# Kernel optimization log

Hardware: AMD Instinct MI355X
Metric: run time of the kernel (lower is better)

## Reference

```python
import jax, jax.numpy as jnp
import numpy as np

B, T, D, H, K = 4, 2048, 512, 8, 31
INNER = 2048  # dim * ff_mult
DH = D // H   # 64
EPS = 1e-5

def _ln(x, g, b):
    m = jnp.mean(x, axis=-1, keepdims=True)
    v = jnp.var(x, axis=-1, keepdims=True)
    return (x - m) * jax.lax.rsqrt(v + EPS) * g + b

def _ff(x, g, b, w1, b1, w2, b2):
    h = jax.nn.silu(_ln(x, g, b) @ w1 + b1)
    return h @ w2 + b2

def _rope_cos_sin(t, dh, theta=10000.0):
    freqs = 1.0 / theta ** (jnp.arange(0, dh, 2, dtype=jnp.float32) / dh)
    ang = jnp.arange(t, dtype=jnp.float32)[:, None] * freqs[None, :]
    return jnp.cos(ang), jnp.sin(ang)

def _rotate(x, cos, sin):
    # x: [B,T,H,DH]; complex rotation on (even, odd) pairs, matches torch view_as_complex
    xr = x.reshape(x.shape[:-1] + (DH // 2, 2))
    xe, xo = xr[..., 0], xr[..., 1]
    c, s = cos[None, :, None, :], sin[None, :, None, :]
    return jnp.stack([xe * c - xo * s, xe * s + xo * c], axis=-1).reshape(x.shape)

def setup_inputs():
    ks = iter(jax.random.split(jax.random.key(0), 16))
    w = lambda *s: jax.random.normal(next(ks), s, jnp.float32) * 0.02
    ones = lambda n: jnp.ones((n,), jnp.float32)
    zeros = lambda n: jnp.zeros((n,), jnp.float32)
    return dict(
        x=jax.random.normal(next(ks), (B, T, D), jnp.float32),
        ff1_lng=ones(D), ff1_lnb=zeros(D),
        ff1_w1=w(D, INNER), ff1_b1=zeros(INNER), ff1_w2=w(INNER, D), ff1_b2=zeros(D),
        attn_lng=ones(D), attn_lnb=zeros(D),
        wq=w(D, D), wk=w(D, D), wv=w(D, D), wo=w(D, D),
        conv_lng=ones(D), conv_lnb=zeros(D),
        pw1_w=w(D, 2 * D), pw1_b=zeros(2 * D),
        dw_w=w(D, K), dw_b=zeros(D),
        bn_g=ones(D), bn_b=zeros(D),
        pw2_w=w(D, D), pw2_b=zeros(D),
        ff2_lng=ones(D), ff2_lnb=zeros(D),
        ff2_w1=w(D, INNER), ff2_b1=zeros(INNER), ff2_w2=w(INNER, D), ff2_b2=zeros(D),
        out_lng=ones(D), out_lnb=zeros(D),
    )

def reference(x, ff1_lng, ff1_lnb, ff1_w1, ff1_b1, ff1_w2, ff1_b2,
              attn_lng, attn_lnb, wq, wk, wv, wo,
              conv_lng, conv_lnb, pw1_w, pw1_b, dw_w, dw_b, bn_g, bn_b, pw2_w, pw2_b,
              ff2_lng, ff2_lnb, ff2_w1, ff2_b1, ff2_w2, ff2_b2,
              out_lng, out_lnb):
    # ff1 half-step
    x = x + 0.5 * _ff(x, ff1_lng, ff1_lnb, ff1_w1, ff1_b1, ff1_w2, ff1_b2)
    # RoPE MHSA
    h = _ln(x, attn_lng, attn_lnb)
    q = (h @ wq).reshape(B, T, H, DH)
    k = (h @ wk).reshape(B, T, H, DH)
    v = (h @ wv).reshape(B, T, H, DH)
    cos, sin = _rope_cos_sin(T, DH)
    q, k = _rotate(q, cos, sin), _rotate(k, cos, sin)
    scores = jnp.einsum('bqhd,bkhd->bhqk', q, k) / np.float32(np.sqrt(DH))
    o = jnp.einsum('bhqk,bkhd->bqhd', jax.nn.softmax(scores, axis=-1), v).reshape(B, T, D)
    x = x + o @ wo
    # Conformer conv module
    h = _ln(x, conv_lng, conv_lnb) @ pw1_w + pw1_b         # pointwise1 -> [B,T,2D]
    h = h[..., :D] * jax.nn.sigmoid(h[..., D:])            # GLU over channels
    h = h.transpose(0, 2, 1)                               # [B,D,T]
    h = jax.lax.conv_general_dilated(h, dw_w[:, None, :], (1,), [(K // 2, K // 2)],
                                     dimension_numbers=('NCH', 'OIH', 'NCH'),
                                     feature_group_count=D) + dw_b[None, :, None]
    mu = jnp.mean(h, axis=(0, 2), keepdims=True)           # training-mode BatchNorm1d
    var = jnp.var(h, axis=(0, 2), keepdims=True)
    h = (h - mu) * jax.lax.rsqrt(var + EPS) * bn_g[None, :, None] + bn_b[None, :, None]
    h = jax.nn.silu(h).transpose(0, 2, 1) @ pw2_w + pw2_b  # pointwise2 -> [B,T,D]
    x = x + h
    # ff2 half-step + final LN
    x = x + 0.5 * _ff(x, ff2_lng, ff2_lnb, ff2_w1, ff2_b1, ff2_w2, ff2_b2)
    return _ln(x, out_lng, out_lnb)
```

## Files before the change

### kernel.cpp

```cpp
#include <hip/hip_runtime.h>


typedef float  f32x4   __attribute__((ext_vector_type(4)));
typedef float  f32x16  __attribute__((ext_vector_type(16)));
typedef __bf16 bf16_t;
typedef __bf16 bf16x8  __attribute__((ext_vector_type(8)));
typedef unsigned short u16;
typedef unsigned short u16x4 __attribute__((ext_vector_type(4)));
typedef unsigned short u16x8 __attribute__((ext_vector_type(8)));
typedef unsigned int   u32x4 __attribute__((ext_vector_type(4)));

#define DEVI __device__ __forceinline__

static constexpr int CB = 4, CT = 2048, CD = 512, CH = 8, CDH = 64, CINNER = 2048, CK = 31;
static constexpr int CBT = CB * CT;

DEVI u16 f2bf(float f) {
  unsigned u = __builtin_bit_cast(unsigned, f);
  u += 0x7FFFu + ((u >> 16) & 1u);
  return (u16)(u >> 16);
}
DEVI float bf2f(u16 h) { return __builtin_bit_cast(float, (unsigned)h << 16); }
DEVI float sigm(float x) { return 1.0f / (1.0f + __expf(-x)); }

#if defined(__has_builtin)
#if __has_builtin(__builtin_amdgcn_exp2f)
#define FEX2(x) __builtin_amdgcn_exp2f(x)
#endif
#endif
#ifndef FEX2
DEVI float fex2_asm(float x) {
  float r;
  asm("v_exp_f32 %0, %1\n\ts_nop 1" : "=v"(r) : "v"(x));
  return r;
}
#define FEX2(x) fex2_asm(x)
#endif

DEVI unsigned cvtpk(float lo, float hi) {
  unsigned r;
  asm("v_cvt_pk_bf16_f32 %0, %1, %2" : "=v"(r) : "v"(lo), "v"(hi));
  return r;
}

DEVI void gload16(const bf16_t* g, bf16_t* l) {
  __builtin_amdgcn_global_load_lds(
      (const __attribute__((address_space(1))) unsigned int*)g,
      (__attribute__((address_space(3))) unsigned int*)l, 16, 0, 0);
}

DEVI void pipe_wait(int t, int nt) {
  if (t + 3 <= nt)      asm volatile("s_waitcnt vmcnt(12)" ::: "memory");
  else if (t + 2 == nt) asm volatile("s_waitcnt vmcnt(6)" ::: "memory");
  else                  asm volatile("s_waitcnt vmcnt(0)" ::: "memory");
}

enum { EPI_BF = 0, EPI_SILU_BF = 1, EPI_RES = 2, EPI_GLU = 3, EPI_QKV = 4, EPI_RESF = 5 };

template<int EPI>
__global__ __launch_bounds__(512) void gemm8(
    const bf16_t* __restrict__ A, const bf16_t* __restrict__ B,
    const float* __restrict__ bias, const float* __restrict__ res,
    void* __restrict__ Cv,
    int lda, int ldb, int ldc, int Kd, float scale)
{
  __shared__ __align__(16) bf16_t As[3][256 * 64];
  __shared__ __align__(16) bf16_t Bs[3][128 * 64];

  const int gx = gridDim.x;
  const int nwg = gx * gridDim.y;
  int wg = blockIdx.y * gx + blockIdx.x;
  wg = (wg & 7) * (nwg >> 3) + (wg >> 3);
  const int m0 = (wg / gx) * 256, n0 = (wg % gx) * 128;

  const int tid = threadIdx.x;
  const int wid = tid >> 6, lane = tid & 63;
  const int lrow = lane & 15, lk = lane >> 4;
  const int wm = (wid >> 1) * 64, wn = (wid & 1) * 64;
  const int r = tid >> 3;
  const int cs = (((tid & 7) ^ (r & 7)) << 3);
  const int fsw = lrow & 7;

  auto stage = [&](int kt, int s) {
    const bf16_t* ga = A + (long)(m0 + r) * lda + (kt * 64 + cs);
    const bf16_t* gb = B + (long)(n0 + r) * ldb + (kt * 64 + cs);
    bf16_t* as = &As[s][0];
    bf16_t* bs = &Bs[s][0];
#pragma unroll
    for (int it = 0; it < 4; ++it)
      gload16(ga + (long)it * 64 * lda, as + tid * 8 + it * 4096);
#pragma unroll
    for (int it = 0; it < 2; ++it)
      gload16(gb + (long)it * 64 * ldb, bs + tid * 8 + it * 4096);
  };

  f32x4 acc[4][4] = {};
  const int nt = Kd / 64;

  stage(0, 0);
  stage(1, 1);
  stage(2, 2);

  int s = 0;
  for (int t = 0; t < nt; ++t) {
    pipe_wait(t, nt);
    asm volatile("s_barrier" ::: "memory");

    bf16x8 av[2][4], bv[2][4];
    const bf16_t* as = &As[s][0];
    const bf16_t* bs = &Bs[s][0];
#pragma unroll
    for (int kk = 0; kk < 2; ++kk) {
#pragma unroll
      for (int i = 0; i < 4; ++i)
        av[kk][i] = *(const bf16x8*)&as[(wm + i * 16 + lrow) * 64 + ((((kk << 2) + lk) ^ fsw) << 3)];
#pragma unroll
      for (int j = 0; j < 4; ++j)
        bv[kk][j] = *(const bf16x8*)&bs[(wn + j * 16 + lrow) * 64 + ((((kk << 2) + lk) ^ fsw) << 3)];
    }
    __builtin_amdgcn_s_setprio(1);
#pragma unroll
    for (int kk = 0; kk < 2; ++kk)
#pragma unroll
      for (int i = 0; i < 4; ++i)
#pragma unroll
        for (int j = 0; j < 4; ++j)
          acc[i][j] = __builtin_amdgcn_mfma_f32_16x16x32_bf16(av[kk][i], bv[kk][j], acc[i][j], 0, 0, 0);
    __builtin_amdgcn_s_setprio(0);

    asm volatile("s_barrier" ::: "memory");
    if (t + 3 < nt) stage(t + 3, s);
    s = (s == 2) ? 0 : s + 1;
  }

  if constexpr (EPI == EPI_GLU) {
#pragma unroll
    for (int jp = 0; jp < 2; ++jp) {
      int oc = ((n0 + wn) >> 1) + jp * 16 + lrow;
      float ba = bias[oc], bb = bias[512 + oc];
#pragma unroll
      for (int i = 0; i < 4; ++i) {
#pragma unroll
        for (int rr = 0; rr < 4; ++rr) {
          int row = m0 + wm + i * 16 + lk * 4 + rr;
          float av_ = acc[i][2 * jp][rr] + ba;
          float bv_ = acc[i][2 * jp + 1][rr] + bb;
          ((bf16_t*)Cv)[(long)row * ldc + oc] = (bf16_t)(av_ * sigm(bv_));
        }
      }
    }
  } else if constexpr (EPI == EPI_QKV) {
    bf16_t* vt = (bf16_t*)res;
    const float2* cst = (const float2*)bias;
    const float SC = 0.125f * 1.44269504089f;
#pragma unroll
    for (int j = 0; j < 4; ++j) {
      int col = n0 + wn + j * 16 + lrow;
      if (col < 1024) {
        int ip = (col & 63) >> 1;
        bool odd = (col & 1) != 0;
        bool isQ = col < 512;
#pragma unroll
        for (int i = 0; i < 4; ++i) {
#pragma unroll
          for (int rr = 0; rr < 4; ++rr) {
            int row = m0 + wm + i * 16 + lk * 4 + rr;
            float2 csv = cst[(row & (CT - 1)) * 32 + ip];
            float mine = acc[i][j][rr];
            float other = __shfl_xor(mine, 1);
            float v = odd ? (other * csv.y + mine * csv.x)
                          : (mine * csv.x - other * csv.y);
            if (isQ) v *= SC;
            ((bf16_t*)Cv)[(long)row * ldc + col] = (bf16_t)v;
          }
        }
      } else {
        int dg = col - 1024;
        int hh = dg >> 6, d = dg & 63;
#pragma unroll
        for (int i = 0; i < 4; ++i) {
          int row0 = m0 + wm + i * 16 + lk * 4;
          int b = row0 >> 11, t = row0 & 2047;
          u16x4 pk;
#pragma unroll
          for (int rr = 0; rr < 4; ++rr) pk[rr] = f2bf(acc[i][j][rr]);
          *(u16x4*)(vt + ((long)(b * 8 + hh) * 64 + d) * 2048 + t) = pk;
        }
      }
    }
  } else {
#pragma unroll
    for (int j = 0; j < 4; ++j) {
      int col = n0 + wn + j * 16 + lrow;
      float bb = bias ? bias[col] : 0.0f;
#pragma unroll
      for (int i = 0; i < 4; ++i) {
#pragma unroll
        for (int rr = 0; rr < 4; ++rr) {
          int row = m0 + wm + i * 16 + lk * 4 + rr;
          long idx = (long)row * ldc + col;
          float v = (acc[i][j][rr] + bb) * scale;
          if constexpr (EPI == EPI_SILU_BF) v *= sigm(v);
          ((bf16_t*)Cv)[idx] = (bf16_t)v;
        }
      }
    }
  }
}

template<int BM, int BN, int BK, int EPI>
__global__ __launch_bounds__(256) void gemm_bf(
    const bf16_t* __restrict__ A, const bf16_t* __restrict__ B,
    const float* __restrict__ bias, const float* __restrict__ res,
    void* __restrict__ Cv,
    int lda, int ldb, int ldc, int Kd, float scale)
{
  __shared__ __align__(16) bf16_t As[BM * BK];
  __shared__ __align__(16) bf16_t Bs[BN * BK];

  const int gx = gridDim.x;
  const int nwg = gx * gridDim.y;
  int wg = blockIdx.y * gx + blockIdx.x;
  wg = (wg & 7) * (nwg >> 3) + (wg >> 3);
  const int m0 = (wg / gx) * BM, n0 = (wg % gx) * BN;

  const int tid = threadIdx.x;
  const int wid = tid >> 6, lane = tid & 63;
  const int lrow = lane & 15, lk = lane >> 4;
  constexpr int FM = BM / 32, FN = BN / 32;
  constexpr int NK = BK / 32;
  constexpr int TPR = BK / 8;
  constexpr int RPP = 256 / TPR;
  const int wm = (wid >> 1) * (BM / 2), wn = (wid & 1) * (BN / 2);
  const int r = tid / TPR;
  const int cs = (((tid & (TPR - 1)) ^ (r & 7)) << 3);
  const int fsw = lrow & 7;

  f32x4 acc[FM][FN] = {};

  for (int k0 = 0; k0 < Kd; k0 += BK) {
    const bf16_t* ga = A + (long)(m0 + r) * lda + (k0 + cs);
    const bf16_t* gb = B + (long)(n0 + r) * ldb + (k0 + cs);
#pragma unroll
    for (int it = 0; it < BM / RPP; ++it)
      gload16(ga + (long)it * RPP * lda, &As[tid * 8 + it * 2048]);
#pragma unroll
    for (int it = 0; it < BN / RPP; ++it)
      gload16(gb + (long)it * RPP * ldb, &Bs[tid * 8 + it * 2048]);
    __syncthreads();

    bf16x8 av[NK][FM], bv[NK][FN];
#pragma unroll
    for (int kk = 0; kk < NK; ++kk) {
#pragma unroll
      for (int i = 0; i < FM; ++i)
        av[kk][i] = *(const bf16x8*)&As[(wm + i * 16 + lrow) * BK + ((((kk << 2) + lk) ^ fsw) << 3)];
#pragma unroll
      for (int j = 0; j < FN; ++j)
        bv[kk][j] = *(const bf16x8*)&Bs[(wn + j * 16 + lrow) * BK + ((((kk << 2) + lk) ^ fsw) << 3)];
    }
#pragma unroll
    for (int kk = 0; kk < NK; ++kk)
#pragma unroll
      for (int i = 0; i < FM; ++i)
#pragma unroll
        for (int j = 0; j < FN; ++j)
          acc[i][j] = __builtin_amdgcn_mfma_f32_16x16x32_bf16(av[kk][i], bv[kk][j], acc[i][j], 0, 0, 0);
    __syncthreads();
  }

#pragma unroll
  for (int j = 0; j < FN; ++j) {
    int col = n0 + wn + j * 16 + lrow;
    float bb = bias ? bias[col] : 0.0f;
#pragma unroll
    for (int i = 0; i < FM; ++i) {
#pragma unroll
      for (int rr = 0; rr < 4; ++rr) {
        int row = m0 + wm + i * 16 + lk * 4 + rr;
        long idx = (long)row * ldc + col;
        float v = (acc[i][j][rr] + bb) * scale;
        if constexpr (EPI == EPI_SILU_BF) v *= sigm(v);
        if constexpr (EPI == EPI_RES) {
          ((bf16_t*)Cv)[idx] = (bf16_t)(bf2f(((const u16*)res)[idx]) + v);
        } else if constexpr (EPI == EPI_RESF) {
          ((bf16_t*)Cv)[idx] = (bf16_t)(res[idx] + v);
        } else {
          ((bf16_t*)Cv)[idx] = (bf16_t)v;
        }
      }
    }
  }
}

__global__ __launch_bounds__(512) void fattn_k(
    const bf16_t* __restrict__ QK,
    const bf16_t* __restrict__ VT,
    bf16_t* __restrict__ O)
{
  __shared__ __align__(16) bf16_t S[32768];

  const int tid = threadIdx.x;
  const int w = tid >> 6, lane = tid & 63;
  const int l31 = lane & 31, hi = lane >> 5;
  const int q0 = blockIdx.x * 256;
  const int bh = blockIdx.y, b = bh >> 3, h = bh & 7;

  const int r8 = tid >> 3;
  const int csw = ((tid & 7) ^ (r8 & 7)) << 3;
  const int fswl = l31 & 7;

  const bf16_t* Qg = QK + ((long)b * CT + q0) * 1536 + h * 64;
  const bf16_t* Kg = QK + (long)b * CT * 1536 + 512 + h * 64;
  const bf16_t* Vg = VT + (long)bh * 64 * 2048;

#pragma unroll
  for (int it = 0; it < 4; ++it)
    gload16(Qg + (long)(r8 + it * 64) * 1536 + csw, &S[16384 + tid * 8 + it * 4096]);
  gload16(Kg + (long)r8 * 1536 + csw, &S[tid * 8]);
  gload16(Vg + (long)r8 * 2048 + csw, &S[4096 + tid * 8]);
  __syncthreads();

  bf16x8 qb[4];
#pragma unroll
  for (int m = 0; m < 4; ++m)
    qb[m] = *(const bf16x8*)&S[16384 + (w * 32 + l31) * 64 + (((m * 2 + hi) ^ fswl) << 3)];

  const u16x8 onesu = {0x3F80, 0x3F80, 0x3F80, 0x3F80, 0x3F80, 0x3F80, 0x3F80, 0x3F80};
  const bf16x8 onesf = __builtin_bit_cast(bf16x8, onesu);

  f32x16 o0 = {}, o1 = {}, lacc = {};

#define FA_BODY(CURK, CURV, NXTK, NXTV, KV0, STG)                               \
  {                                                                             \
    if (STG) {                                                                  \
      const int nxt = (KV0) + 64;                                               \
      gload16(Kg + (long)(nxt + r8) * 1536 + csw, &S[(NXTK) + tid * 8]);        \
      gload16(Vg + (long)r8 * 2048 + nxt + csw, &S[(NXTV) + tid * 8]);          \
    }                                                                           \
    bf16x8 ka[2][4];                                                            \
    _Pragma("unroll")                                                           \
    for (int j = 0; j < 2; ++j)                                                 \
      _Pragma("unroll")                                                         \
      for (int m = 0; m < 4; ++m)                                               \
        ka[j][m] = *(const bf16x8*)&S[(CURK) + (j * 32 + l31) * 64 +            \
                                      (((m * 2 + hi) ^ fswl) << 3)];            \
    f32x16 s0 = {}, s1 = {};                                                    \
    __builtin_amdgcn_s_setprio(1);                                              \
    _Pragma("unroll")                                                           \
    for (int m = 0; m < 4; ++m) {                                               \
      s0 = __builtin_amdgcn_mfma_f32_32x32x16_bf16(ka[0][m], qb[m], s0, 0, 0, 0); \
      s1 = __builtin_amdgcn_mfma_f32_32x32x16_bf16(ka[1][m], qb[m], s1, 0, 0, 0); \
    }                                                                           \
    __builtin_amdgcn_s_setprio(0);                                              \
    _Pragma("unroll")                                                           \
    for (int rr = 0; rr < 16; ++rr) s0[rr] = FEX2(s0[rr]);                      \
    _Pragma("unroll")                                                           \
    for (int rr = 0; rr < 16; ++rr) s1[rr] = FEX2(s1[rr]);                      \
    bf16x8 pw[4];                                                               \
    _Pragma("unroll")                                                           \
    for (int jk = 0; jk < 4; ++jk) {                                            \
      float e0, e1, e2, e3, e4, e5, e6, e7;                                     \
      if (jk == 0) { e0=s0[0];e1=s0[1];e2=s0[2];e3=s0[3];e4=s0[4];e5=s0[5];e6=s0[6];e7=s0[7]; }        \
      else if (jk == 1) { e0=s0[8];e1=s0[9];e2=s0[10];e3=s0[11];e4=s0[12];e5=s0[13];e6=s0[14];e7=s0[15]; } \
      else if (jk == 2) { e0=s1[0];e1=s1[1];e2=s1[2];e3=s1[3];e4=s1[4];e5=s1[5];e6=s1[6];e7=s1[7]; }   \
      else { e0=s1[8];e1=s1[9];e2=s1[10];e3=s1[11];e4=s1[12];e5=s1[13];e6=s1[14];e7=s1[15]; }          \
      unsigned a0 = cvtpk(e0, e1), a1 = cvtpk(e2, e3);                          \
      unsigned b0 = cvtpk(e4, e5), b1 = cvtpk(e6, e7);                          \
      asm("v_permlane32_swap_b32 %0, %1" : "+v"(a0), "+v"(b0));                 \
      asm("v_permlane32_swap_b32 %0, %1" : "+v"(a1), "+v"(b1));                 \
      u32x4 t; t[0] = a0; t[1] = a1; t[2] = b0; t[3] = b1;                      \
      pw[jk] = __builtin_bit_cast(bf16x8, t);                                   \
    }                                                                           \
    bf16x8 va[2][4];                                                            \
    _Pragma("unroll")                                                           \
    for (int n = 0; n < 2; ++n)                                                 \
      _Pragma("unroll")                                                         \
      for (int jk = 0; jk < 4; ++jk)                                            \
        va[n][jk] = *(const bf16x8*)&S[(CURV) + (n * 32 + l31) * 64 +           \
                                       (((jk * 2 + hi) ^ fswl) << 3)];          \
    __builtin_amdgcn_s_setprio(1);                                              \
    _Pragma("unroll")                                                           \
    for (int jk = 0; jk < 4; ++jk) {                                            \
      o0 = __builtin_amdgcn_mfma_f32_32x32x16_bf16(va[0][jk], pw[jk], o0, 0, 0, 0); \
      o1 = __builtin_amdgcn_mfma_f32_32x32x16_bf16(va[1][jk], pw[jk], o1, 0, 0, 0); \
      lacc = __builtin_amdgcn_mfma_f32_32x32x16_bf16(onesf, pw[jk], lacc, 0, 0, 0); \
    }                                                                           \
    __builtin_amdgcn_s_setprio(0);                                              \
    __syncthreads();                                                            \
  }

  for (int kv0 = 0; kv0 < CT; kv0 += 128) {
    FA_BODY(0, 4096, 8192, 12288, kv0, 1)
    FA_BODY(8192, 12288, 0, 4096, kv0 + 64, (kv0 + 128 < CT))
  }
#undef FA_BODY

  float rl = 1.0f / lacc[0];
  bf16_t* Op = O + ((long)b * CT + q0 + w * 32 + l31) * CD + h * 64;
#pragma unroll
  for (int n = 0; n < 2; ++n) {
#pragma unroll
    for (int m = 0; m < 4; ++m) {
      u16x4 pk4;
#pragma unroll
      for (int e = 0; e < 4; ++e)
        pk4[e] = f2bf((n ? o1[m * 4 + e] : o0[m * 4 + e]) * rl);
      *(u16x4*)(Op + n * 32 + m * 8 + hi * 4) = pk4;
    }
  }
}

DEVI void wtrans_dev(const float* w, u16* o, int Kd, int N, int bx, int by,
                     int tid, u16 (*lt)[72])
{
  const int k0 = by * 64, n0 = bx * 64;
#pragma unroll
  for (int it = 0; it < 4; ++it) {
    int kk = (tid >> 4) + it * 16, nn = (tid & 15) * 4;
    float4 f = *(const float4*)(w + (long)(k0 + kk) * N + n0 + nn);
    lt[kk][nn + 0] = f2bf(f.x); lt[kk][nn + 1] = f2bf(f.y);
    lt[kk][nn + 2] = f2bf(f.z); lt[kk][nn + 3] = f2bf(f.w);
  }
  __syncthreads();
#pragma unroll
  for (int it = 0; it < 2; ++it) {
    int nn = (tid >> 3) + it * 32, kk = (tid & 7) * 8;
    u16x8 pk;
#pragma unroll
    for (int e = 0; e < 8; ++e) pk[e] = lt[kk + e][nn];
    *(u16x8*)(o + (long)(n0 + nn) * Kd + k0 + kk) = pk;
  }
}

DEVI void pwtrans_dev(const float* w, u16* o, int bx, int by, int tid,
                      u16 (*lt)[72])
{
  const int k0 = by * 64, n0 = bx * 64;
#pragma unroll
  for (int it = 0; it < 4; ++it) {
    int kk = (tid >> 4) + it * 16, nn = (tid & 15) * 4;
    float4 f = *(const float4*)(w + (long)(k0 + kk) * 1024 + n0 + nn);
    lt[kk][nn + 0] = f2bf(f.x); lt[kk][nn + 1] = f2bf(f.y);
    lt[kk][nn + 2] = f2bf(f.z); lt[kk][nn + 3] = f2bf(f.w);
  }
  __syncthreads();
#pragma unroll
  for (int it = 0; it < 2; ++it) {
    int nn = (tid >> 3) + it * 32, kk = (tid & 7) * 8;
    int s = n0 + nn;
    int d = ((s & 511) >> 4) * 32 + (s >> 9) * 16 + (s & 15);
    u16x8 pk;
#pragma unroll
    for (int e = 0; e < 8; ++e) pk[e] = lt[kk + e][nn];
    *(u16x8*)(o + (long)d * 512 + k0 + kk) = pk;
  }
}

__global__ __launch_bounds__(256) void prep_k(
    const float* ff1_w1, const float* ff1_w2,
    const float* wq, const float* wk, const float* wv, const float* wo,
    const float* pw1_w, const float* pw2_w,
    const float* ff2_w1, const float* ff2_w2, const float* dw_w,
    u16* w_ff1a, u16* w_ff1b, u16* w_qkv, u16* w_o, u16* w_pw1, u16* w_pw2,
    u16* w_ff2a, u16* w_ff2b, float* dwT, float2* ropeT)
{
  __shared__ u16 lt[64][72];
  const int r = blockIdx.x;
  const int tid = threadIdx.x;

  if (r < 256) {
    wtrans_dev(ff1_w1, w_ff1a, 512, 2048, r & 31, r >> 5, tid, lt);
  } else if (r < 512) {
    int r2 = r - 256;
    wtrans_dev(ff1_w2, w_ff1b, 2048, 512, r2 & 7, r2 >> 3, tid, lt);
  } else if (r < 576) {
    int r2 = r - 512;
    wtrans_dev(wq, w_qkv, 512, 512, r2 & 7, r2 >> 3, tid, lt);
  } else if (r < 640) {
    int r2 = r - 576;
    wtrans_dev(wk, w_qkv + (size_t)512 * 512, 512, 512, r2 & 7, r2 >> 3, tid, lt);
  } else if (r < 704) {
    int r2 = r - 640;
    wtrans_dev(wv, w_qkv + (size_t)1024 * 512, 512, 512, r2 & 7, r2 >> 3, tid, lt);
  } else if (r < 768) {
    int r2 = r - 704;
    wtrans_dev(wo, w_o, 512, 512, r2 & 7, r2 >> 3, tid, lt);
  } else if (r < 896) {
    int r2 = r - 768;
    pwtrans_dev(pw1_w, w_pw1, r2 & 15, r2 >> 4, tid, lt);
  } else if (r < 960) {
    int r2 = r - 896;
    wtrans_dev(pw2_w, w_pw2, 512, 512, r2 & 7, r2 >> 3, tid, lt);
  } else if (r < 1216) {
    int r2 = r - 960;
    wtrans_dev(ff2_w1, w_ff2a, 512, 2048, r2 & 31, r2 >> 5, tid, lt);
  } else if (r < 1472) {
    int r2 = r - 1216;
    wtrans_dev(ff2_w2, w_ff2b, 2048, 512, r2 & 7, r2 >> 3, tid, lt);
  } else if (r < 1534) {
    int i = (r - 1472) * 256 + tid;
    if (i < 512 * 31) { int c = i / 31, k = i % 31; dwT[k * 512 + c] = dw_w[i]; }
  } else {
    int i = (r - 1534) * 256 + tid;
    int t = i >> 5, ip = i & 31;
    float freq = __expf(-(float)ip * (9.210340371976184f / 32.0f));
    float ang = (float)t * freq;
    ropeT[i] = make_float2(cosf(ang), sinf(ang));
  }
}

template<int IBF, int OBF>
__global__ __launch_bounds__(256) void ln_k(
    const void* __restrict__ in, const float* __restrict__ g,
    const float* __restrict__ b, void* __restrict__ out)
{
  const int w = threadIdx.x >> 6, lane = threadIdx.x & 63;
  const long row = (long)blockIdx.x * 4 + w;
  float v[8];
  if (IBF) {
    u16x8 u = ((const u16x8*)in)[row * 64 + lane];
#pragma unroll
    for (int e = 0; e < 8; ++e) v[e] = bf2f(u[e]);
  } else {
    float4 f0 = ((const float4*)in)[row * 128 + lane * 2];
    float4 f1 = ((const float4*)in)[row * 128 + lane * 2 + 1];
    v[0] = f0.x; v[1] = f0.y; v[2] = f0.z; v[3] = f0.w;
    v[4] = f1.x; v[5] = f1.y; v[6] = f1.z; v[7] = f1.w;
  }
  float s = 0, q = 0;
#pragma unroll
  for (int e = 0; e < 8; ++e) { s += v[e]; q += v[e] * v[e]; }
#pragma unroll
  for (int o = 32; o; o >>= 1) { s += __shfl_xor(s, o); q += __shfl_xor(q, o); }
  float mean = s * (1.0f / CD);
  float var = q * (1.0f / CD) - mean * mean;
  float rstd = rsqrtf(var + 1e-5f);
  float4 g0 = ((const float4*)g)[lane * 2], g1 = ((const float4*)g)[lane * 2 + 1];
  float4 b0 = ((const float4*)b)[lane * 2], b1 = ((const float4*)b)[lane * 2 + 1];
  float gg[8] = {g0.x, g0.y, g0.z, g0.w, g1.x, g1.y, g1.z, g1.w};
  float bb[8] = {b0.x, b0.y, b0.z, b0.w, b1.x, b1.y, b1.z, b1.w};
  float o8[8];
#pragma unroll
  for (int e = 0; e < 8; ++e) o8[e] = (v[e] - mean) * rstd * gg[e] + bb[e];
  if (OBF) {
    u16x8 pk;
#pragma unroll
    for (int e = 0; e < 8; ++e) pk[e] = f2bf(o8[e]);
    ((u16x8*)out)[row * 64 + lane] = pk;
  } else {
    ((float4*)out)[row * 128 + lane * 2] = make_float4(o8[0], o8[1], o8[2], o8[3]);
    ((float4*)out)[row * 128 + lane * 2 + 1] = make_float4(o8[4], o8[5], o8[6], o8[7]);
  }
}

__global__ __launch_bounds__(256) void dwconv_k(
    const u16* __restrict__ in, const float* __restrict__ wT,
    const float* __restrict__ wb, u16* __restrict__ out)
{
  long idx = (long)blockIdx.x * 256 + threadIdx.x;
  int c4 = (int)(idx & 127) * 4;
  int t0 = (int)((idx >> 7) & 255) * 8;
  int b = (int)(idx >> 15);
  const u16* base = in + (long)b * CT * CD;
  float4 bias = *(const float4*)(wb + c4);
  float4 acc[8];
#pragma unroll
  for (int t = 0; t < 8; ++t) acc[t] = bias;
#pragma unroll
  for (int j = 0; j < 38; ++j) {
    int tr = t0 + j - 15;
    float4 row = make_float4(0.f, 0.f, 0.f, 0.f);
    if (tr >= 0 && tr < CT) {
      u16x4 rv = *(const u16x4*)(base + (long)tr * CD + c4);
      row = make_float4(bf2f(rv[0]), bf2f(rv[1]), bf2f(rv[2]), bf2f(rv[3]));
    }
#pragma unroll
    for (int t = 0; t < 8; ++t) {
      int k = j - t;
      if (k >= 0 && k < CK) {
        float4 w4 = *(const float4*)(wT + k * CD + c4);
        acc[t].x += row.x * w4.x; acc[t].y += row.y * w4.y;
        acc[t].z += row.z * w4.z; acc[t].w += row.w * w4.w;
      }
    }
  }
#pragma unroll
  for (int t = 0; t < 8; ++t) {
    u16x4 pk;
    pk[0] = f2bf(acc[t].x); pk[1] = f2bf(acc[t].y);
    pk[2] = f2bf(acc[t].z); pk[3] = f2bf(acc[t].w);
    *(u16x4*)(out + ((long)b * CT + t0 + t) * CD + c4) = pk;
  }
}

__global__ __launch_bounds__(256) void bn_part_k(
    const u16* __restrict__ in, float* __restrict__ psum, float* __restrict__ psq)
{
  const int blk = blockIdx.x;
  const int tid = threadIdx.x;
  const int c0 = tid, c1 = tid + 256;
  const int rows = CBT / 256;
  const u16* base = in + (long)blk * rows * CD;
  float s0 = 0, q0 = 0, s1 = 0, q1 = 0;
  for (int r = 0; r < rows; ++r) {
    float v0 = bf2f(base[(long)r * CD + c0]); s0 += v0; q0 += v0 * v0;
    float v1 = bf2f(base[(long)r * CD + c1]); s1 += v1; q1 += v1 * v1;
  }
  psum[blk * CD + c0] = s0; psq[blk * CD + c0] = q0;
  psum[blk * CD + c1] = s1; psq[blk * CD + c1] = q1;
}

__global__ __launch_bounds__(256) void bn_fin_k(
    const float* __restrict__ psum, const float* __restrict__ psq,
    float* __restrict__ stat)
{
  int c = blockIdx.x * 256 + threadIdx.x;
  float s = 0, q = 0;
  for (int i = 0; i < 256; ++i) { s += psum[i * CD + c]; q += psq[i * CD + c]; }
  float mean = s * (1.0f / CBT);
  float var = q * (1.0f / CBT) - mean * mean;
  stat[c] = mean;
  stat[CD + c] = rsqrtf(var + 1e-5f);
}

__global__ __launch_bounds__(256) void bn_app_k(
    const u16* __restrict__ h, const float* __restrict__ stat,
    const float* __restrict__ g, const float* __restrict__ b,
    u16* __restrict__ out)
{
  long idx = (long)blockIdx.x * 256 + threadIdx.x;
  int c = (int)(idx & 511);
  float v = (bf2f(h[idx]) - stat[c]) * stat[CD + c] * g[c] + b[c];
  v = v * sigm(v);
  out[idx] = f2bf(v);
}

extern "C" void kernel_launch(void* const* d_in, const int* in_sizes, int n_in,
                              void* d_out, int out_size, void* d_ws, size_t ws_size,
                              hipStream_t stream)
{
  const float* x        = (const float*)d_in[0];
  const float* ff1_lng  = (const float*)d_in[1];
  const float* ff1_lnb  = (const float*)d_in[2];
  const float* ff1_w1   = (const float*)d_in[3];
  const float* ff1_b1   = (const float*)d_in[4];
  const float* ff1_w2   = (const float*)d_in[5];
  const float* ff1_b2   = (const float*)d_in[6];
  const float* attn_lng = (const float*)d_in[7];
  const float* attn_lnb = (const float*)d_in[8];
  const float* wq       = (const float*)d_in[9];
  const float* wk       = (const float*)d_in[10];
  const float* wv       = (const float*)d_in[11];
  const float* wo       = (const float*)d_in[12];
  const float* conv_lng = (const float*)d_in[13];
  const float* conv_lnb = (const float*)d_in[14];
  const float* pw1_w    = (const float*)d_in[15];
  const float* pw1_b    = (const float*)d_in[16];
  const float* dw_w     = (const float*)d_in[17];
  const float* dw_b     = (const float*)d_in[18];
  const float* bn_g     = (const float*)d_in[19];
  const float* bn_b     = (const float*)d_in[20];
  const float* pw2_w    = (const float*)d_in[21];
  const float* pw2_b    = (const float*)d_in[22];
  const float* ff2_lng  = (const float*)d_in[23];
  const float* ff2_lnb  = (const float*)d_in[24];
  const float* ff2_w1   = (const float*)d_in[25];
  const float* ff2_b1   = (const float*)d_in[26];
  const float* ff2_w2   = (const float*)d_in[27];
  const float* ff2_b2   = (const float*)d_in[28];
  const float* out_lng  = (const float*)d_in[29];
  const float* out_lnb  = (const float*)d_in[30];
  float* out = (float*)d_out;

  char* p = (char*)d_ws;
  auto alloc = [&](size_t bytes) { char* r = p; p += (bytes + 255) & ~(size_t)255; return r; };
  bf16_t* bufX   = (bf16_t*)alloc((size_t)CBT * CD * 2);
  bf16_t* bufH   = (bf16_t*)alloc((size_t)CBT * CD * 2);
  bf16_t* bufQKV = (bf16_t*)alloc((size_t)CBT * 1536 * 2);
  bf16_t* bufO   = (bf16_t*)alloc((size_t)CBT * CD * 2);
  bf16_t* bufVT  = (bf16_t*)alloc((size_t)CBT * CD * 2);
  bf16_t* bufP   = (bf16_t*)alloc((size_t)CBT * CINNER * 2);
  bf16_t* w_ff1a = (bf16_t*)alloc((size_t)CD * CINNER * 2);
  bf16_t* w_ff1b = (bf16_t*)alloc((size_t)CD * CINNER * 2);
  bf16_t* w_qkv  = (bf16_t*)alloc((size_t)CD * 1536 * 2);
  bf16_t* w_o    = (bf16_t*)alloc((size_t)CD * CD * 2);
  bf16_t* w_pw1  = (bf16_t*)alloc((size_t)CD * 2 * CD * 2);
  bf16_t* w_pw2  = (bf16_t*)alloc((size_t)CD * CD * 2);
  bf16_t* w_ff2a = (bf16_t*)alloc((size_t)CD * CINNER * 2);
  bf16_t* w_ff2b = (bf16_t*)alloc((size_t)CD * CINNER * 2);
  float* dwT  = (float*)alloc((size_t)CK * CD * 4);
  float2* ropeT = (float2*)alloc((size_t)CT * 32 * 8);
  float* psum = (float*)alloc((size_t)256 * CD * 4);
  float* psq  = (float*)alloc((size_t)256 * CD * 4);
  float* stat = (float*)alloc((size_t)2 * CD * 4);

  const dim3 blk(256);
  const dim3 blk8(512);

  prep_k<<<dim3(1790), blk, 0, stream>>>(
      ff1_w1, ff1_w2, wq, wk, wv, wo, pw1_w, pw2_w, ff2_w1, ff2_w2, dw_w,
      (u16*)w_ff1a, (u16*)w_ff1b, (u16*)w_qkv, (u16*)w_o, (u16*)w_pw1,
      (u16*)w_pw2, (u16*)w_ff2a, (u16*)w_ff2b, dwT, ropeT);

  ln_k<0, 1><<<dim3(CBT / 4), blk, 0, stream>>>(x, ff1_lng, ff1_lnb, bufH);
  gemm8<EPI_SILU_BF><<<dim3(16, 32), blk8, 0, stream>>>(
      bufH, w_ff1a, ff1_b1, nullptr, bufP, CD, CD, CINNER, CD, 1.0f);
  gemm_bf<64, 128, 128, EPI_RESF><<<dim3(4, 128), blk, 0, stream>>>(
      bufP, w_ff1b, ff1_b2, x, bufX, CINNER, CINNER, CD, CINNER, 0.5f);

  ln_k<1, 1><<<dim3(CBT / 4), blk, 0, stream>>>(bufX, attn_lng, attn_lnb, bufH);
  gemm8<EPI_QKV><<<dim3(12, 32), blk8, 0, stream>>>(
      bufH, w_qkv, (const float*)ropeT, (const float*)bufVT, bufQKV, CD, CD, 1536, CD, 1.0f);
  fattn_k<<<dim3(CT / 256, CB * CH), blk8, 0, stream>>>(bufQKV, bufVT, bufO);
  gemm_bf<64, 128, 128, EPI_RES><<<dim3(4, 128), blk, 0, stream>>>(
      bufO, w_o, nullptr, (const float*)bufX, bufX, CD, CD, CD, CD, 1.0f);

  ln_k<1, 1><<<dim3(CBT / 4), blk, 0, stream>>>(bufX, conv_lng, conv_lnb, bufH);
  gemm8<EPI_GLU><<<dim3(8, 32), blk8, 0, stream>>>(
      bufH, w_pw1, pw1_b, nullptr, bufH, CD, CD, CD, CD, 1.0f);
  dwconv_k<<<dim3(512), blk, 0, stream>>>((const u16*)bufH, dwT, dw_b, (u16*)bufO);
  bn_part_k<<<dim3(256), blk, 0, stream>>>((const u16*)bufO, psum, psq);
  bn_fin_k<<<dim3(2), blk, 0, stream>>>(psum, psq, stat);
  bn_app_k<<<dim3(CBT * CD / 256), blk, 0, stream>>>((const u16*)bufO, stat, bn_g, bn_b, (u16*)bufH);
  gemm_bf<64, 128, 128, EPI_RES><<<dim3(4, 128), blk, 0, stream>>>(
      bufH, w_pw2, pw2_b, (const float*)bufX, bufX, CD, CD, CD, CD, 1.0f);

  ln_k<1, 1><<<dim3(CBT / 4), blk, 0, stream>>>(bufX, ff2_lng, ff2_lnb, bufH);
  gemm8<EPI_SILU_BF><<<dim3(16, 32), blk8, 0, stream>>>(
      bufH, w_ff2a, ff2_b1, nullptr, bufP, CD, CD, CINNER, CD, 1.0f);
  gemm_bf<64, 128, 128, EPI_RES><<<dim3(4, 128), blk, 0, stream>>>(
      bufP, w_ff2b, ff2_b2, (const float*)bufX, bufX, CINNER, CINNER, CD, CINNER, 0.5f);

  ln_k<1, 0><<<dim3(CBT / 4), blk, 0, stream>>>(bufX, out_lng, out_lnb, out);

  (void)in_sizes; (void)n_in; (void)out_size; (void)ws_size;
}
```

Before: 322.7 us.

## Replace N=512 GEMMs with 128x128 triple-buffered pipelined kernel; widen dwconv

The single-stage gemm_bf used for the four N=512 projections (ff down-projections, attention output, pw2) is replaced by gemm4n, a 512-thread, 128x128-tile kernel with a three-stage global_load_lds pipeline, vmcnt-based waits and MFMA priority boosting, mirroring the existing gemm8. The aim is to hide global-load latency that the old load-sync-compute loop exposed. The grid halves to 256 workgroups, which may reduce occupancy or wave balance on the GPU. Separately, the depthwise conv processes 8 channels per thread with 16-byte loads and stores instead of 4, halving its grid and raising register use.

```diff
diff --git a/kernel.cpp b/kernel.cpp
--- a/kernel.cpp
+++ b/kernel.cpp
@@ -49,9 +49,14 @@
       (__attribute__((address_space(3))) unsigned int*)l, 16, 0, 0);
 }
 
-DEVI void pipe_wait(int t, int nt) {
+DEVI void pipe_wait6(int t, int nt) {
   if (t + 3 <= nt)      asm volatile("s_waitcnt vmcnt(12)" ::: "memory");
   else if (t + 2 == nt) asm volatile("s_waitcnt vmcnt(6)" ::: "memory");
+  else                  asm volatile("s_waitcnt vmcnt(0)" ::: "memory");
+}
+DEVI void pipe_wait4(int t, int nt) {
+  if (t + 3 <= nt)      asm volatile("s_waitcnt vmcnt(8)" ::: "memory");
+  else if (t + 2 == nt) asm volatile("s_waitcnt vmcnt(4)" ::: "memory");
   else                  asm volatile("s_waitcnt vmcnt(0)" ::: "memory");
 }
 
@@ -103,7 +108,7 @@
 
   int s = 0;
   for (int t = 0; t < nt; ++t) {
-    pipe_wait(t, nt);
+    pipe_wait6(t, nt);
     asm volatile("s_barrier" ::: "memory");
 
     bf16x8 av[2][4], bv[2][4];
@@ -208,79 +213,91 @@
   }
 }
 
-template<int BM, int BN, int BK, int EPI>
-__global__ __launch_bounds__(256) void gemm_bf(
+template<int EPI>
+__global__ __launch_bounds__(512) void gemm4n(
     const bf16_t* __restrict__ A, const bf16_t* __restrict__ B,
     const float* __restrict__ bias, const float* __restrict__ res,
     void* __restrict__ Cv,
     int lda, int ldb, int ldc, int Kd, float scale)
 {
-  __shared__ __align__(16) bf16_t As[BM * BK];
-  __shared__ __align__(16) bf16_t Bs[BN * BK];
+  __shared__ __align__(16) bf16_t As[3][128 * 64];
+  __shared__ __align__(16) bf16_t Bs[3][128 * 64];
 
   const int gx = gridDim.x;
   const int nwg = gx * gridDim.y;
   int wg = blockIdx.y * gx + blockIdx.x;
   wg = (wg & 7) * (nwg >> 3) + (wg >> 3);
-  const int m0 = (wg / gx) * BM, n0 = (wg % gx) * BN;
+  const int m0 = (wg / gx) * 128, n0 = (wg % gx) * 128;
 
   const int tid = threadIdx.x;
   const int wid = tid >> 6, lane = tid & 63;
   const int lrow = lane & 15, lk = lane >> 4;
-  constexpr int FM = BM / 32, FN = BN / 32;
-  constexpr int NK = BK / 32;
-  constexpr int TPR = BK / 8;
-  constexpr int RPP = 256 / TPR;
-  const int wm = (wid >> 1) * (BM / 2), wn = (wid & 1) * (BN / 2);
-  const int r = tid / TPR;
-  const int cs = (((tid & (TPR - 1)) ^ (r & 7)) << 3);
+  const int wm = (wid >> 1) * 32, wn = (wid & 1) * 64;
+  const int r = tid >> 3;
+  const int cs = (((tid & 7) ^ (r & 7)) << 3);
   const int fsw = lrow & 7;
 
-  f32x4 acc[FM][FN] = {};
-
-  for (int k0 = 0; k0 < Kd; k0 += BK) {
-    const bf16_t* ga = A + (long)(m0 + r) * lda + (k0 + cs);
-    const bf16_t* gb = B + (long)(n0 + r) * ldb + (k0 + cs);
-#pragma unroll
-    for (int it = 0; it < BM / RPP; ++it)
-      gload16(ga + (long)it * RPP * lda, &As[tid * 8 + it * 2048]);
-#pragma unroll
-    for (int it = 0; it < BN / RPP; ++it)
-      gload16(gb + (long)it * RPP * ldb, &Bs[tid * 8 + it * 2048]);
-    __syncthreads();
-
-    bf16x8 av[NK][FM], bv[NK][FN];
-#pragma unroll
-    for (int kk = 0; kk < NK; ++kk) {
-#pragma unroll
-      for (int i = 0; i < FM; ++i)
-        av[kk][i] = *(const bf16x8*)&As[(wm + i * 16 + lrow) * BK + ((((kk << 2) + lk) ^ fsw) << 3)];
-#pragma unroll
-      for (int j = 0; j < FN; ++j)
-        bv[kk][j] = *(const bf16x8*)&Bs[(wn + j * 16 + lrow) * BK + ((((kk << 2) + lk) ^ fsw) << 3)];
-    }
-#pragma unroll
-    for (int kk = 0; kk < NK; ++kk)
-#pragma unroll
-      for (int i = 0; i < FM; ++i)
-#pragma unroll
-        for (int j = 0; j < FN; ++j)
+  auto stage = [&](int kt, int s) {
+    const bf16_t* ga = A + (long)(m0 + r) * lda + (kt * 64 + cs);
+    const bf16_t* gb = B + (long)(n0 + r) * ldb + (kt * 64 + cs);
+#pragma unroll
+    for (int it = 0; it < 2; ++it)
+      gload16(ga + (long)it * 64 * lda, &As[s][tid * 8 + it * 4096]);
+#pragma unroll
+    for (int it = 0; it < 2; ++it)
+      gload16(gb + (long)it * 64 * ldb, &Bs[s][tid * 8 + it * 4096]);
+  };
+
+  f32x4 acc[2][4] = {};
+  const int nt = Kd / 64;
+
+  stage(0, 0);
+  stage(1, 1);
+  stage(2, 2);
+
+  int s = 0;
+  for (int t = 0; t < nt; ++t) {
+    pipe_wait4(t, nt);
+    asm volatile("s_barrier" ::: "memory");
+
+    bf16x8 av[2][2], bv[2][4];
+    const bf16_t* as = &As[s][0];
+    const bf16_t* bs = &Bs[s][0];
+#pragma unroll
+    for (int kk = 0; kk < 2; ++kk) {
+#pragma unroll
+      for (int i = 0; i < 2; ++i)
+        av[kk][i] = *(const bf16x8*)&as[(wm + i * 16 + lrow) * 64 + ((((kk << 2) + lk) ^ fsw) << 3)];
+#pragma unroll
+      for (int j = 0; j < 4; ++j)
+        bv[kk][j] = *(const bf16x8*)&bs[(wn + j * 16 + lrow) * 64 + ((((kk << 2) + lk) ^ fsw) << 3)];
+    }
+    __builtin_amdgcn_s_setprio(1);
+#pragma unroll
+    for (int kk = 0; kk < 2; ++kk)
+#pragma unroll
+      for (int i = 0; i < 2; ++i)
+#pragma unroll
+        for (int j = 0; j < 4; ++j)
           acc[i][j] = __builtin_amdgcn_mfma_f32_16x16x32_bf16(av[kk][i], bv[kk][j], acc[i][j], 0, 0, 0);
-    __syncthreads();
-  }
-
-#pragma unroll
-  for (int j = 0; j < FN; ++j) {
+    __builtin_amdgcn_s_setprio(0);
+
+    asm volatile("s_barrier" ::: "memory");
+    if (t + 3 < nt) stage(t + 3, s);
+    s = (s == 2) ? 0 : s + 1;
+  }
+
+#pragma unroll
+  for (int j = 0; j < 4; ++j) {
     int col = n0 + wn + j * 16 + lrow;
     float bb = bias ? bias[col] : 0.0f;
 #pragma unroll
-    for (int i = 0; i < FM; ++i) {
+    for (int i = 0; i < 2; ++i) {
 #pragma unroll
       for (int rr = 0; rr < 4; ++rr) {
         int row = m0 + wm + i * 16 + lk * 4 + rr;
         long idx = (long)row * ldc + col;
         float v = (acc[i][j][rr] + bb) * scale;
-        if constexpr (EPI == EPI_SILU_BF) v *= sigm(v);
         if constexpr (EPI == EPI_RES) {
           ((bf16_t*)Cv)[idx] = (bf16_t)(bf2f(((const u16*)res)[idx]) + v);
         } else if constexpr (EPI == EPI_RESF) {
@@ -559,38 +576,46 @@
     const float* __restrict__ wb, u16* __restrict__ out)
 {
   long idx = (long)blockIdx.x * 256 + threadIdx.x;
-  int c4 = (int)(idx & 127) * 4;
-  int t0 = (int)((idx >> 7) & 255) * 8;
-  int b = (int)(idx >> 15);
+  int c8 = (int)(idx & 63) * 8;
+  int t0 = (int)((idx >> 6) & 255) * 8;
+  int b = (int)(idx >> 14);
   const u16* base = in + (long)b * CT * CD;
-  float4 bias = *(const float4*)(wb + c4);
-  float4 acc[8];
-#pragma unroll
-  for (int t = 0; t < 8; ++t) acc[t] = bias;
+  float bias8[8];
+#pragma unroll
+  for (int e = 0; e < 8; ++e) bias8[e] = wb[c8 + e];
+  float acc[8][8];
+#pragma unroll
+  for (int t = 0; t < 8; ++t)
+#pragma unroll
+    for (int e = 0; e < 8; ++e) acc[t][e] = bias8[e];
 #pragma unroll
   for (int j = 0; j < 38; ++j) {
     int tr = t0 + j - 15;
-    float4 row = make_float4(0.f, 0.f, 0.f, 0.f);
+    float row[8];
     if (tr >= 0 && tr < CT) {
-      u16x4 rv = *(const u16x4*)(base + (long)tr * CD + c4);
-      row = make_float4(bf2f(rv[0]), bf2f(rv[1]), bf2f(rv[2]), bf2f(rv[3]));
+      u16x8 rv = *(const u16x8*)(base + (long)tr * CD + c8);
+#pragma unroll
+      for (int e = 0; e < 8; ++e) row[e] = bf2f(rv[e]);
+    } else {
+#pragma unroll
+      for (int e = 0; e < 8; ++e) row[e] = 0.0f;
     }
 #pragma unroll
     for (int t = 0; t < 8; ++t) {
       int k = j - t;
       if (k >= 0 && k < CK) {
-        float4 w4 = *(const float4*)(wT + k * CD + c4);
-        acc[t].x += row.x * w4.x; acc[t].y += row.y * w4.y;
-        acc[t].z += row.z * w4.z; acc[t].w += row.w * w4.w;
+        const float* wr = wT + k * CD + c8;
+#pragma unroll
+        for (int e = 0; e < 8; ++e) acc[t][e] += row[e] * wr[e];
       }
     }
   }
 #pragma unroll
   for (int t = 0; t < 8; ++t) {
-    u16x4 pk;
-    pk[0] = f2bf(acc[t].x); pk[1] = f2bf(acc[t].y);
-    pk[2] = f2bf(acc[t].z); pk[3] = f2bf(acc[t].w);
-    *(u16x4*)(out + ((long)b * CT + t0 + t) * CD + c4) = pk;
+    u16x8 pk;
+#pragma unroll
+    for (int e = 0; e < 8; ++e) pk[e] = f2bf(acc[t][e]);
+    *(u16x8*)(out + ((long)b * CT + t0 + t) * CD + c8) = pk;
   }
 }
 
@@ -706,30 +731,30 @@
   ln_k<0, 1><<<dim3(CBT / 4), blk, 0, stream>>>(x, ff1_lng, ff1_lnb, bufH);
   gemm8<EPI_SILU_BF><<<dim3(16, 32), blk8, 0, stream>>>(
       bufH, w_ff1a, ff1_b1, nullptr, bufP, CD, CD, CINNER, CD, 1.0f);
-  gemm_bf<64, 128, 128, EPI_RESF><<<dim3(4, 128), blk, 0, stream>>>(
+  gemm4n<EPI_RESF><<<dim3(4, 64), blk8, 0, stream>>>(
       bufP, w_ff1b, ff1_b2, x, bufX, CINNER, CINNER, CD, CINNER, 0.5f);
 
   ln_k<1, 1><<<dim3(CBT / 4), blk, 0, stream>>>(bufX, attn_lng, attn_lnb, bufH);
   gemm8<EPI_QKV><<<dim3(12, 32), blk8, 0, stream>>>(
       bufH, w_qkv, (const float*)ropeT, (const float*)bufVT, bufQKV, CD, CD, 1536, CD, 1.0f);
   fattn_k<<<dim3(CT / 256, CB * CH), blk8, 0, stream>>>(bufQKV, bufVT, bufO);
-  gemm_bf<64, 128, 128, EPI_RES><<<dim3(4, 128), blk, 0, stream>>>(
+  gemm4n<EPI_RES><<<dim3(4, 64), blk8, 0, stream>>>(
       bufO, w_o, nullptr, (const float*)bufX, bufX, CD, CD, CD, CD, 1.0f);
 
   ln_k<1, 1><<<dim3(CBT / 4), blk, 0, stream>>>(bufX, conv_lng, conv_lnb, bufH);
   gemm8<EPI_GLU><<<dim3(8, 32), blk8, 0, stream>>>(
       bufH, w_pw1, pw1_b, nullptr, bufH, CD, CD, CD, CD, 1.0f);
-  dwconv_k<<<dim3(512), blk, 0, stream>>>((const u16*)bufH, dwT, dw_b, (u16*)bufO);
+  dwconv_k<<<dim3(256), blk, 0, stream>>>((const u16*)bufH, dwT, dw_b, (u16*)bufO);
   bn_part_k<<<dim3(256), blk, 0, stream>>>((const u16*)bufO, psum, psq);
   bn_fin_k<<<dim3(2), blk, 0, stream>>>(psum, psq, stat);
   bn_app_k<<<dim3(CBT * CD / 256), blk, 0, stream>>>((const u16*)bufO, stat, bn_g, bn_b, (u16*)bufH);
-  gemm_bf<64, 128, 128, EPI_RES><<<dim3(4, 128), blk, 0, stream>>>(
+  gemm4n<EPI_RES><<<dim3(4, 64), blk8, 0, stream>>>(
       bufH, w_pw2, pw2_b, (const float*)bufX, bufX, CD, CD, CD, CD, 1.0f);
 
   ln_k<1, 1><<<dim3(CBT / 4), blk, 0, stream>>>(bufX, ff2_lng, ff2_lnb, bufH);
   gemm8<EPI_SILU_BF><<<dim3(16, 32), blk8, 0, stream>>>(
       bufH, w_ff2a, ff2_b1, nullptr, bufP, CD, CD, CINNER, CD, 1.0f);
-  gemm_bf<64, 128, 128, EPI_RES><<<dim3(4, 128), blk, 0, stream>>>(
+  gemm4n<EPI_RES><<<dim3(4, 64), blk8, 0, stream>>>(
       bufP, w_ff2b, ff2_b2, (const float*)bufX, bufX, CINNER, CINNER, CD, CINNER, 0.5f);
 
   ln_k<1, 0><<<dim3(CBT / 4), blk, 0, stream>>>(bufX, out_lng, out_lnb, out);
```

Result: slower. 336.2 us (+4.2%).
